# Optimization experiments

Hardware: AMD Instinct MI355X
Metric: run time of the kernel (lower is better)

Reference implementation:

```python
import jax, jax.numpy as jnp
import numpy as np

N_NODES = 50000
N_EDGES = 800000
VOCAB = 4096          # node_emb_size
EMB_DIM = 128         # node_emb_dim
HIDDEN = 128          # hidden_dim -> layer1 out = 2*HIDDEN
N_POS = 1024


def gcn_conv(h, edge_index, W, b, n):
    """PyG GCNConv: lin -> add self loops -> sym-normalized scatter-add -> +bias."""
    h = h @ W                                   # [N, out]
    row, col = edge_index[0], edge_index[1]     # source, target
    loop = jnp.arange(n)
    row = jnp.concatenate([row, loop])
    col = jnp.concatenate([col, loop])
    deg = jax.ops.segment_sum(jnp.ones(row.shape[0], dtype=h.dtype), col, num_segments=n)
    dinv = jnp.where(deg > 0, jax.lax.rsqrt(deg), 0.0)
    norm = dinv[row] * dinv[col]                # [E+N]
    msg = h[row] * norm[:, None]                # gather + scale
    return jax.ops.segment_sum(msg, col, num_segments=n) + b


def setup_inputs() -> dict:
    key = jax.random.key(0)
    ks = jax.random.split(key, 10)
    x = jax.random.randint(ks[0], (N_NODES, 1), 0, VOCAB)
    edge_index = jax.random.randint(ks[1], (2, N_EDGES), 0, N_NODES)
    x_position = jax.random.randint(ks[2], (N_POS,), 0, N_NODES)
    # Embedding init: normal(0, emb_dim^-0.5) per initialize_parameters
    emb = jax.random.normal(ks[3], (VOCAB, EMB_DIM), jnp.float32) * EMB_DIM ** -0.5
    # GCN / linear weights (glorot-ish)
    W1 = jax.random.normal(ks[4], (EMB_DIM, 2 * HIDDEN), jnp.float32) * (EMB_DIM ** -0.5)
    b1 = jnp.zeros((2 * HIDDEN,), jnp.float32)
    W2 = jax.random.normal(ks[5], (2 * HIDDEN, HIDDEN), jnp.float32) * ((2 * HIDDEN) ** -0.5)
    b2 = jnp.zeros((HIDDEN,), jnp.float32)
    Wc = jax.random.normal(ks[6], (HIDDEN, VOCAB), jnp.float32) * (HIDDEN ** -0.5)
    bc = jnp.zeros((VOCAB,), jnp.float32)
    return {"x": x, "edge_index": edge_index, "x_position": x_position,
            "emb": emb, "W1": W1, "b1": b1, "W2": W2, "b2": b2, "Wc": Wc, "bc": bc}


def reference(x, edge_index, x_position, emb, W1, b1, W2, b2, Wc, bc):
    n = x.shape[0]
    h = emb[x[:, 0]]                                   # Embedding + squeeze(1)
    h = jax.nn.relu(gcn_conv(h, edge_index, W1, b1, n))
    z = gcn_conv(h, edge_index, W2, b2, n)             # [N, HIDDEN]
    logits = z @ Wc + bc                               # classifier over all nodes
    # embedding stage: mean of classified rows at x_position, keep dim 0
    return jnp.mean(logits[x_position], axis=0, keepdims=True)  # [1, VOCAB]
```

## Files before the change

kernel.cpp:

```cpp
#include <hip/hip_runtime.h>

constexpr int EMB  = 128;
constexpr int H1D  = 256;
constexpr int H2D  = 128;
constexpr int VOC  = 4096;
constexpr int NSL  = 32;

__global__ void k_init(int* cnt, int* count, unsigned int* flagbits, unsigned int* markw,
                       float* wagg, float* wsum, int* nflag, int* total,
                       int n, int nwords) {
    int i = blockIdx.x * blockDim.x + threadIdx.x;
    if (i < n) { cnt[i] = 0; count[i] = 0; wagg[i] = 0.0f; }
    if (i < nwords) { flagbits[i] = 0u; markw[i] = 0u; }
    if (i < NSL * H1D) wsum[i] = 0.0f;
    if (i == 0) { *nflag = 0; *total = 0; }
}

constexpr int RPB = 16;
__global__ void k_embW1C(const float* __restrict__ emb, const float* __restrict__ W1,
                         float* __restrict__ embW1,
                         const int* __restrict__ xpos, int* count,
                         unsigned int* flagbits, int np) {
    int t = threadIdx.x;
    if (blockIdx.x == VOC / RPB) {
        for (int p = t; p < np; p += blockDim.x) {
            int v = xpos[p];
            atomicAdd(&count[v], 1);
            atomicOr(&flagbits[v >> 5], 1u << (v & 31));
        }
        return;
    }
    __shared__ float er[RPB][EMB];
    int r0 = blockIdx.x * RPB;
    for (int i = t; i < RPB * EMB; i += 256) {
        er[i / EMB][i % EMB] = emb[(size_t)r0 * EMB + i];
    }
    __syncthreads();
    float acc[RPB];
#pragma unroll
    for (int rr = 0; rr < RPB; rr++) acc[rr] = 0.0f;
    for (int k = 0; k < EMB; k++) {
        float w = W1[k * H1D + t];
#pragma unroll
        for (int rr = 0; rr < RPB; rr++) acc[rr] += er[rr][k] * w;
    }
#pragma unroll
    for (int rr = 0; rr < RPB; rr++) {
        embW1[(size_t)(r0 + rr) * H1D + t] = acc[rr];
    }
}

__global__ void k_hist(const int* __restrict__ row, const int* __restrict__ col,
                       const unsigned int* __restrict__ flagbits, int* cnt,
                       unsigned int* markw, int ne) {
    int e = blockIdx.x * blockDim.x + threadIdx.x;
    if (e < ne) {
        int c = col[e];
        atomicAdd(&cnt[c], 1);
        if ((flagbits[c >> 5] >> (c & 31)) & 1u) {
            int r = row[e];
            atomicOr(&markw[r >> 5], 1u << (r & 31));
        }
    }
}

__global__ void k_alloc(unsigned int* needw,
                        const unsigned int* __restrict__ flagbits,
                        const int* __restrict__ cnt, const int* __restrict__ count,
                        float* wagg, int* needlist, int* nflag, int* total,
                        int* offs, int* cursor, int n) {
    int v = blockIdx.x * blockDim.x + threadIdx.x;
    int lane = threadIdx.x & 63;
    int cv = 0;
    bool need = false;
    if (v < n) {
        cv = cnt[v];
        bool mark = (needw[v >> 5] >> (v & 31)) & 1u;
        bool flag = (flagbits[v >> 5] >> (v & 31)) & 1u;
        need = mark || flag;
        if (flag) wagg[v] = (float)count[v] / ((float)cv + 1.0f);
    }
    unsigned long long nm = __ballot(need);
    int wbase = (v & ~63) >> 5;
    if (lane == 0)  needw[wbase]     = (unsigned int)(nm & 0xffffffffu);
    if (lane == 32) needw[wbase + 1] = (unsigned int)(nm >> 32);
    int seg = need ? cv : 0;
    int incl = seg;
#pragma unroll
    for (int d = 1; d < 64; d <<= 1) {
        int t = __shfl_up(incl, d);
        if (lane >= d) incl += t;
    }
    int excl = incl - seg;
    int wave_total = __shfl(incl, 63);
    int rank = __popcll(nm & ((1ull << lane) - 1));
    int wcnt = __popcll(nm);
    int base_id = 0, base_off = 0;
    if (lane == 0) {
        if (wcnt > 0) base_id = atomicAdd(nflag, wcnt);
        if (wave_total > 0) base_off = atomicAdd(total, wave_total);
    }
    base_id  = __shfl(base_id, 0);
    base_off = __shfl(base_off, 0);
    if (need) {
        needlist[base_id + rank] = v;
        int o = base_off + excl;
        offs[v] = o;
        cursor[v] = o;
    }
}

__global__ void k_scatter(const int* __restrict__ row, const int* __restrict__ col,
                          const unsigned int* __restrict__ needw,
                          const unsigned int* __restrict__ flagbits,
                          const int* __restrict__ count,
                          const int* __restrict__ x, const int* __restrict__ cnt,
                          int* cursor, int2* srowp, float* wagg, int ne) {
    int e = blockIdx.x * blockDim.x + threadIdx.x;
    if (e < ne) {
        int c = col[e];
        if ((needw[c >> 5] >> (c & 31)) & 1u) {
            int r = row[e];
            int pos = atomicAdd(&cursor[c], 1);
            float dr = rsqrtf((float)cnt[r] + 1.0f);
            int2 pk; pk.x = x[r]; pk.y = __float_as_int(dr);
            srowp[pos] = pk;
            if ((flagbits[c >> 5] >> (c & 31)) & 1u) {
                float dc = rsqrtf((float)cnt[c] + 1.0f);
                atomicAdd(&wagg[r], (float)count[c] * dc * dr);
            }
        }
    }
}

__global__ void k_fconv(const int* __restrict__ needlist, const int* __restrict__ nneed_p,
                        const float* __restrict__ wagg, const int* __restrict__ x,
                        const int2* __restrict__ srowp,
                        const int* __restrict__ offs, const int* __restrict__ cnt,
                        const float* __restrict__ embW1, const float* __restrict__ b1,
                        float* __restrict__ wsum) {
    int lane = threadIdx.x & 63;
    int wib  = threadIdx.x >> 6;
    int wid  = blockIdx.x * (blockDim.x >> 6) + wib;
    int nw   = gridDim.x * (blockDim.x >> 6);
    int nn   = *nneed_p;
    const float4* __restrict__ ew = (const float4*)embW1;
    float4 bfrag = ((const float4*)b1)[lane];
    float4 acc2 = {0.0f, 0.0f, 0.0f, 0.0f};

    for (int i = wid; i < nn; i += nw) {
        int v = needlist[i];
        int cv = cnt[v];
        float dv = rsqrtf((float)cv + 1.0f);
        float wa = wagg[v];
        float4 s = ew[(size_t)x[v] * 64 + lane];
        float w0 = dv * dv;
        float4 acc;
        acc.x = bfrag.x + w0 * s.x;
        acc.y = bfrag.y + w0 * s.y;
        acc.z = bfrag.z + w0 * s.z;
        acc.w = bfrag.w + w0 * s.w;
        int start = offs[v], m = cv;
        for (int base = 0; base < m; base += 64) {
            int mm = min(64, m - base);
            int xr = 0; float wr = 0.0f;
            if (lane < mm) {
                int2 pk = srowp[start + base + lane];
                xr = pk.x;
                wr = __int_as_float(pk.y) * dv;
            }
            int e = 0;
            for (; e + 4 <= mm; e += 4) {
                int i0 = __shfl(xr, e),     i1 = __shfl(xr, e + 1);
                int i2 = __shfl(xr, e + 2), i3 = __shfl(xr, e + 3);
                float q0 = __shfl(wr, e),     q1 = __shfl(wr, e + 1);
                float q2 = __shfl(wr, e + 2), q3 = __shfl(wr, e + 3);
                float4 t0 = ew[(size_t)i0 * 64 + lane];
                float4 t1 = ew[(size_t)i1 * 64 + lane];
                float4 t2 = ew[(size_t)i2 * 64 + lane];
                float4 t3 = ew[(size_t)i3 * 64 + lane];
                acc.x += q0 * t0.x + q1 * t1.x + q2 * t2.x + q3 * t3.x;
                acc.y += q0 * t0.y + q1 * t1.y + q2 * t2.y + q3 * t3.y;
                acc.z += q0 * t0.z + q1 * t1.z + q2 * t2.z + q3 * t3.z;
                acc.w += q0 * t0.w + q1 * t1.w + q2 * t2.w + q3 * t3.w;
            }
            for (; e < mm; e++) {
                int i0 = __shfl(xr, e);
                float q0 = __shfl(wr, e);
                float4 t0 = ew[(size_t)i0 * 64 + lane];
                acc.x += q0 * t0.x;
                acc.y += q0 * t0.y;
                acc.z += q0 * t0.z;
                acc.w += q0 * t0.w;
            }
        }
        acc2.x += wa * fmaxf(acc.x, 0.0f);
        acc2.y += wa * fmaxf(acc.y, 0.0f);
        acc2.z += wa * fmaxf(acc.z, 0.0f);
        acc2.w += wa * fmaxf(acc.w, 0.0f);
    }

    __shared__ float red[4][H1D];
    red[wib][4 * lane + 0] = acc2.x;
    red[wib][4 * lane + 1] = acc2.y;
    red[wib][4 * lane + 2] = acc2.z;
    red[wib][4 * lane + 3] = acc2.w;
    __syncthreads();
    int t = threadIdx.x;
    float ssum = red[0][t] + red[1][t] + red[2][t] + red[3][t];
    atomicAdd(&wsum[(blockIdx.x & (NSL - 1)) * H1D + t], ssum);
}

__global__ void k_zout(const float* __restrict__ wsum, const float* __restrict__ W2,
                       const float* __restrict__ b2, const float* __restrict__ Wc,
                       const float* __restrict__ bc, float* __restrict__ out,
                       float inv_np) {
    __shared__ float ws[H1D];
    __shared__ float z[H2D];
    int t = threadIdx.x;
    float s = 0.0f;
#pragma unroll
    for (int c = 0; c < NSL; c++) s += wsum[c * H1D + t];
    ws[t] = s;
    __syncthreads();
    if (t < H2D) {
        float acc = 0.0f;
#pragma unroll 8
        for (int k = 0; k < H1D; k++) acc += ws[k] * W2[k * H2D + t];
        z[t] = b2[t] + acc * inv_np;
    }
    __syncthreads();
    int c = blockIdx.x * blockDim.x + t;
    float acc = bc[c];
#pragma unroll 8
    for (int j = 0; j < H2D; j++) acc += z[j] * Wc[(size_t)j * VOC + c];
    out[c] = acc;
}

extern "C" void kernel_launch(void* const* d_in, const int* in_sizes, int n_in,
                              void* d_out, int out_size, void* d_ws, size_t ws_size,
                              hipStream_t stream) {
    const int n  = in_sizes[0];
    const int ne = in_sizes[1] / 2;
    const int np = in_sizes[2];

    const int*   x    = (const int*)d_in[0];
    const int*   ei   = (const int*)d_in[1];
    const int*   xpos = (const int*)d_in[2];
    const float* emb  = (const float*)d_in[3];
    const float* W1   = (const float*)d_in[4];
    const float* b1   = (const float*)d_in[5];
    const float* W2   = (const float*)d_in[6];
    const float* b2   = (const float*)d_in[7];
    const float* Wc   = (const float*)d_in[8];
    const float* bc   = (const float*)d_in[9];
    float*       out  = (float*)d_out;

    const int* row = ei;
    const int* col = ei + ne;

    char* p = (char*)d_ws;
    auto alloc = [&](size_t bytes) {
        char* r = p;
        p += (bytes + 255) & ~(size_t)255;
        return r;
    };
    const int nb     = (n + 255) / 256;
    const int neb    = (ne + 255) / 256;
    const int nwords = nb * 8;

    int*          cnt      = (int*)alloc((size_t)n * 4);
    int*          offs     = (int*)alloc((size_t)n * 4);
    int*          cursor   = (int*)alloc((size_t)n * 4);
    int*          count    = (int*)alloc((size_t)n * 4);
    int*          needlist = (int*)alloc((size_t)n * 4);
    unsigned int* needw    = (unsigned int*)alloc((size_t)nwords * 4);
    unsigned int* flagbits = (unsigned int*)alloc((size_t)nwords * 4);
    int2*         srowp    = (int2*)alloc((size_t)ne * 8);
    int*          nflag    = (int*)alloc(256 * 4);
    int*          total    = (int*)alloc(256 * 4);
    float*        wagg     = (float*)alloc((size_t)n * 4);
    float*        embW1    = (float*)alloc((size_t)VOC * H1D * 4);
    float*        wsum     = (float*)alloc((size_t)NSL * H1D * 4);

    k_init<<<nb, 256, 0, stream>>>(cnt, count, flagbits, needw, wagg, wsum,
                                   nflag, total, n, nwords);
    k_embW1C<<<VOC / RPB + 1, 256, 0, stream>>>(emb, W1, embW1, xpos, count, flagbits, np);
    k_hist<<<neb, 256, 0, stream>>>(row, col, flagbits, cnt, needw, ne);
    k_alloc<<<nb, 256, 0, stream>>>(needw, flagbits, cnt, count, wagg,
                                    needlist, nflag, total, offs, cursor, n);
    k_scatter<<<neb, 256, 0, stream>>>(row, col, needw, flagbits, count, x, cnt,
                                       cursor, srowp, wagg, ne);
    k_fconv<<<2048, 256, 0, stream>>>(needlist, nflag, wagg, x, srowp, offs, cnt,
                                      embW1, b1, wsum);
    k_zout<<<VOC / 256, 256, 0, stream>>>(wsum, W2, b2, Wc, bc, out, 1.0f / (float)np);
}
```

Before: 192.6 us.

## Fuse init into precompute kernel, vectorize edge passes, precompute per-node packed degree

Merges the zero-init kernel into the embedding×W1 precompute kernel, so one launch does both, and has a single block clear count/flagbits before the x_position histogram. The edge-histogram and scatter kernels now process four edges per thread using int4 loads of row/col. A per-node packed (x, rsqrt degree) array is built in k_alloc so scatter and fconv read one int2 instead of recomputing rsqrt and gathering x and cnt separately. The intent is fewer launches and fewer scattered loads, at the cost of an extra n*8-byte buffer and a serial single-block clear of count and flagbits.

```diff
diff --git a/kernel.cpp b/kernel.cpp
--- a/kernel.cpp
+++ b/kernel.cpp
@@ -5,61 +5,84 @@
 constexpr int H2D  = 128;
 constexpr int VOC  = 4096;
 constexpr int NSL  = 32;
-
-__global__ void k_init(int* cnt, int* count, unsigned int* flagbits, unsigned int* markw,
-                       float* wagg, float* wsum, int* nflag, int* total,
-                       int n, int nwords) {
-    int i = blockIdx.x * blockDim.x + threadIdx.x;
-    if (i < n) { cnt[i] = 0; count[i] = 0; wagg[i] = 0.0f; }
-    if (i < nwords) { flagbits[i] = 0u; markw[i] = 0u; }
-    if (i < NSL * H1D) wsum[i] = 0.0f;
-    if (i == 0) { *nflag = 0; *total = 0; }
-}
-
-constexpr int RPB = 16;
-__global__ void k_embW1C(const float* __restrict__ emb, const float* __restrict__ W1,
-                         float* __restrict__ embW1,
-                         const int* __restrict__ xpos, int* count,
-                         unsigned int* flagbits, int np) {
+constexpr int RPB  = 16;
+
+__global__ void k_pre(const float* __restrict__ emb, const float* __restrict__ W1,
+                      float* __restrict__ embW1,
+                      const int* __restrict__ xpos, int* count, unsigned int* flagbits,
+                      int* cnt, unsigned int* needw, float* wagg, float* wsum,
+                      int* nflag, int* total, int np, int n, int nwords) {
     int t = threadIdx.x;
-    if (blockIdx.x == VOC / RPB) {
-        for (int p = t; p < np; p += blockDim.x) {
+    int b = blockIdx.x;
+    if (b < VOC / RPB) {
+        __shared__ float er[RPB][EMB];
+        int r0 = b * RPB;
+        for (int i = t; i < RPB * EMB; i += 256) {
+            er[i / EMB][i % EMB] = emb[(size_t)r0 * EMB + i];
+        }
+        __syncthreads();
+        float acc[RPB];
+#pragma unroll
+        for (int rr = 0; rr < RPB; rr++) acc[rr] = 0.0f;
+        for (int k = 0; k < EMB; k++) {
+            float w = W1[k * H1D + t];
+#pragma unroll
+            for (int rr = 0; rr < RPB; rr++) acc[rr] += er[rr][k] * w;
+        }
+#pragma unroll
+        for (int rr = 0; rr < RPB; rr++) {
+            embW1[(size_t)(r0 + rr) * H1D + t] = acc[rr];
+        }
+        return;
+    }
+    if (b == VOC / RPB) {
+        for (int i = t; i < n; i += 256) count[i] = 0;
+        for (int i = t; i < nwords; i += 256) flagbits[i] = 0u;
+        __syncthreads();
+        for (int p = t; p < np; p += 256) {
             int v = xpos[p];
             atomicAdd(&count[v], 1);
             atomicOr(&flagbits[v >> 5], 1u << (v & 31));
         }
         return;
     }
-    __shared__ float er[RPB][EMB];
-    int r0 = blockIdx.x * RPB;
-    for (int i = t; i < RPB * EMB; i += 256) {
-        er[i / EMB][i % EMB] = emb[(size_t)r0 * EMB + i];
-    }
-    __syncthreads();
-    float acc[RPB];
-#pragma unroll
-    for (int rr = 0; rr < RPB; rr++) acc[rr] = 0.0f;
-    for (int k = 0; k < EMB; k++) {
-        float w = W1[k * H1D + t];
-#pragma unroll
-        for (int rr = 0; rr < RPB; rr++) acc[rr] += er[rr][k] * w;
-    }
-#pragma unroll
-    for (int rr = 0; rr < RPB; rr++) {
-        embW1[(size_t)(r0 + rr) * H1D + t] = acc[rr];
-    }
+    int i = (b - (VOC / RPB + 1)) * 256 + t;
+    if (i < n) { cnt[i] = 0; wagg[i] = 0.0f; }
+    if (i < nwords) needw[i] = 0u;
+    if (i < NSL * H1D) wsum[i] = 0.0f;
+    if (i == 0) { *nflag = 0; *total = 0; }
 }
 
 __global__ void k_hist(const int* __restrict__ row, const int* __restrict__ col,
                        const unsigned int* __restrict__ flagbits, int* cnt,
                        unsigned int* markw, int ne) {
     int e = blockIdx.x * blockDim.x + threadIdx.x;
-    if (e < ne) {
-        int c = col[e];
-        atomicAdd(&cnt[c], 1);
-        if ((flagbits[c >> 5] >> (c & 31)) & 1u) {
-            int r = row[e];
-            atomicOr(&markw[r >> 5], 1u << (r & 31));
+    int base = e * 4;
+    if (base + 3 < ne) {
+        int4 c4 = ((const int4*)col)[e];
+        atomicAdd(&cnt[c4.x], 1);
+        atomicAdd(&cnt[c4.y], 1);
+        atomicAdd(&cnt[c4.z], 1);
+        atomicAdd(&cnt[c4.w], 1);
+        bool f0 = (flagbits[c4.x >> 5] >> (c4.x & 31)) & 1u;
+        bool f1 = (flagbits[c4.y >> 5] >> (c4.y & 31)) & 1u;
+        bool f2 = (flagbits[c4.z >> 5] >> (c4.z & 31)) & 1u;
+        bool f3 = (flagbits[c4.w >> 5] >> (c4.w & 31)) & 1u;
+        if (f0 | f1 | f2 | f3) {
+            int4 r4 = ((const int4*)row)[e];
+            if (f0) atomicOr(&markw[r4.x >> 5], 1u << (r4.x & 31));
+            if (f1) atomicOr(&markw[r4.y >> 5], 1u << (r4.y & 31));
+            if (f2) atomicOr(&markw[r4.z >> 5], 1u << (r4.z & 31));
+            if (f3) atomicOr(&markw[r4.w >> 5], 1u << (r4.w & 31));
+        }
+    } else {
+        for (int q = base; q < ne; q++) {
+            int c = col[q];
+            atomicAdd(&cnt[c], 1);
+            if ((flagbits[c >> 5] >> (c & 31)) & 1u) {
+                int r = row[q];
+                atomicOr(&markw[r >> 5], 1u << (r & 31));
+            }
         }
     }
 }
@@ -67,6 +90,7 @@
 __global__ void k_alloc(unsigned int* needw,
                         const unsigned int* __restrict__ flagbits,
                         const int* __restrict__ cnt, const int* __restrict__ count,
+                        const int* __restrict__ x, int2* __restrict__ pk,
                         float* wagg, int* needlist, int* nflag, int* total,
                         int* offs, int* cursor, int n) {
     int v = blockIdx.x * blockDim.x + threadIdx.x;
@@ -75,6 +99,9 @@
     bool need = false;
     if (v < n) {
         cv = cnt[v];
+        float dv = rsqrtf((float)cv + 1.0f);
+        int2 p; p.x = x[v]; p.y = __float_as_int(dv);
+        pk[v] = p;
         bool mark = (needw[v >> 5] >> (v & 31)) & 1u;
         bool flag = (flagbits[v >> 5] >> (v & 31)) & 1u;
         need = mark || flag;
@@ -114,27 +141,35 @@
                           const unsigned int* __restrict__ needw,
                           const unsigned int* __restrict__ flagbits,
                           const int* __restrict__ count,
-                          const int* __restrict__ x, const int* __restrict__ cnt,
+                          const int2* __restrict__ pk,
                           int* cursor, int2* srowp, float* wagg, int ne) {
     int e = blockIdx.x * blockDim.x + threadIdx.x;
-    if (e < ne) {
-        int c = col[e];
+    int base = e * 4;
+    auto doedge = [&](int c, int r) {
         if ((needw[c >> 5] >> (c & 31)) & 1u) {
-            int r = row[e];
             int pos = atomicAdd(&cursor[c], 1);
-            float dr = rsqrtf((float)cnt[r] + 1.0f);
-            int2 pk; pk.x = x[r]; pk.y = __float_as_int(dr);
-            srowp[pos] = pk;
+            int2 pr = pk[r];
+            srowp[pos] = pr;
             if ((flagbits[c >> 5] >> (c & 31)) & 1u) {
-                float dc = rsqrtf((float)cnt[c] + 1.0f);
-                atomicAdd(&wagg[r], (float)count[c] * dc * dr);
-            }
-        }
+                float dc = __int_as_float(pk[c].y);
+                atomicAdd(&wagg[r], (float)count[c] * dc * __int_as_float(pr.y));
+            }
+        }
+    };
+    if (base + 3 < ne) {
+        int4 c4 = ((const int4*)col)[e];
+        int4 r4 = ((const int4*)row)[e];
+        doedge(c4.x, r4.x);
+        doedge(c4.y, r4.y);
+        doedge(c4.z, r4.z);
+        doedge(c4.w, r4.w);
+    } else {
+        for (int q = base; q < ne; q++) doedge(col[q], row[q]);
     }
 }
 
 __global__ void k_fconv(const int* __restrict__ needlist, const int* __restrict__ nneed_p,
-                        const float* __restrict__ wagg, const int* __restrict__ x,
+                        const float* __restrict__ wagg, const int2* __restrict__ pk,
                         const int2* __restrict__ srowp,
                         const int* __restrict__ offs, const int* __restrict__ cnt,
                         const float* __restrict__ embW1, const float* __restrict__ b1,
@@ -150,24 +185,24 @@
 
     for (int i = wid; i < nn; i += nw) {
         int v = needlist[i];
-        int cv = cnt[v];
-        float dv = rsqrtf((float)cv + 1.0f);
+        int2 pv = pk[v];
+        float dv = __int_as_float(pv.y);
         float wa = wagg[v];
-        float4 s = ew[(size_t)x[v] * 64 + lane];
+        float4 s = ew[(size_t)pv.x * 64 + lane];
         float w0 = dv * dv;
         float4 acc;
         acc.x = bfrag.x + w0 * s.x;
         acc.y = bfrag.y + w0 * s.y;
         acc.z = bfrag.z + w0 * s.z;
         acc.w = bfrag.w + w0 * s.w;
-        int start = offs[v], m = cv;
+        int start = offs[v], m = cnt[v];
         for (int base = 0; base < m; base += 64) {
             int mm = min(64, m - base);
             int xr = 0; float wr = 0.0f;
             if (lane < mm) {
-                int2 pk = srowp[start + base + lane];
-                xr = pk.x;
-                wr = __int_as_float(pk.y) * dv;
+                int2 pke = srowp[start + base + lane];
+                xr = pke.x;
+                wr = __int_as_float(pke.y) * dv;
             }
             int e = 0;
             for (; e + 4 <= mm; e += 4) {
@@ -266,7 +301,6 @@
         return r;
     };
     const int nb     = (n + 255) / 256;
-    const int neb    = (ne + 255) / 256;
     const int nwords = nb * 8;
 
     int*          cnt      = (int*)alloc((size_t)n * 4);
@@ -276,6 +310,7 @@
     int*          needlist = (int*)alloc((size_t)n * 4);
     unsigned int* needw    = (unsigned int*)alloc((size_t)nwords * 4);
     unsigned int* flagbits = (unsigned int*)alloc((size_t)nwords * 4);
+    int2*         pk       = (int2*)alloc((size_t)n * 8);
     int2*         srowp    = (int2*)alloc((size_t)ne * 8);
     int*          nflag    = (int*)alloc(256 * 4);
     int*          total    = (int*)alloc(256 * 4);
@@ -283,15 +318,18 @@
     float*        embW1    = (float*)alloc((size_t)VOC * H1D * 4);
     float*        wsum     = (float*)alloc((size_t)NSL * H1D * 4);
 
-    k_init<<<nb, 256, 0, stream>>>(cnt, count, flagbits, needw, wagg, wsum,
-                                   nflag, total, n, nwords);
-    k_embW1C<<<VOC / RPB + 1, 256, 0, stream>>>(emb, W1, embW1, xpos, count, flagbits, np);
-    k_hist<<<neb, 256, 0, stream>>>(row, col, flagbits, cnt, needw, ne);
-    k_alloc<<<nb, 256, 0, stream>>>(needw, flagbits, cnt, count, wagg,
+    const int ne4  = (ne + 3) / 4;
+    const int neb4 = (ne4 + 255) / 256;
+
+    k_pre<<<VOC / RPB + 1 + nb, 256, 0, stream>>>(emb, W1, embW1, xpos, count, flagbits,
+                                                  cnt, needw, wagg, wsum, nflag, total,
+                                                  np, n, nwords);
+    k_hist<<<neb4, 256, 0, stream>>>(row, col, flagbits, cnt, needw, ne);
+    k_alloc<<<nb, 256, 0, stream>>>(needw, flagbits, cnt, count, x, pk, wagg,
                                     needlist, nflag, total, offs, cursor, n);
-    k_scatter<<<neb, 256, 0, stream>>>(row, col, needw, flagbits, count, x, cnt,
-                                       cursor, srowp, wagg, ne);
-    k_fconv<<<2048, 256, 0, stream>>>(needlist, nflag, wagg, x, srowp, offs, cnt,
+    k_scatter<<<neb4, 256, 0, stream>>>(row, col, needw, flagbits, count, pk,
+                                        cursor, srowp, wagg, ne);
+    k_fconv<<<2048, 256, 0, stream>>>(needlist, nflag, wagg, pk, srowp, offs, cnt,
                                       embW1, b1, wsum);
     k_zout<<<VOC / 256, 256, 0, stream>>>(wsum, W2, b2, Wc, bc, out, 1.0f / (float)np);
 }
```

Measured after the change: 192.9 us. No clear change (+0.2%).
